# Kernel optimization log

Measured on AMD Instinct MI355X. Metric: run time of the kernel, lower is better.

Reference implementation:

```python
import jax, jax.numpy as jnp
import numpy as np

RADIUS = 0.1
KSIZE = 3          # kernel points per dimension
P_DIM = 3
K = KSIZE ** P_DIM  # 27 kernel points
KP_EXTENT = RADIUS / (KSIZE - 1) * P_DIM ** 0.5


def _kernel_points():
    # grid kernel points, same as getKernelPoints(radius, 3, dim=3)
    xyz = np.linspace(-1.0, 1.0, KSIZE)
    pts = np.meshgrid(*P_DIM * [xyz])
    pts = np.vstack([p.flatten() for p in pts]).T
    pts = pts / P_DIM ** 0.5
    return jnp.asarray(pts * RADIUS, dtype=jnp.float32)  # [K, 3]


def setup_inputs() -> dict:
    key = jax.random.key(0)
    k1, k2, k3, k4, k5 = jax.random.split(key, 5)
    N, S, H, CIN, COUT = 40000, 40000, 32, 64, 64
    # points in a [0, 0.2]^3 cube so neighbor offsets are comparable to radius
    q_pts = jax.random.uniform(k1, (N, 3), jnp.float32) * 0.2
    s_pts = jax.random.uniform(k2, (S, 3), jnp.float32) * 0.2
    neighb_inds = jax.random.randint(k3, (N, H), 0, S)
    x = jax.random.normal(k4, (S, CIN), jnp.float32)
    # kaiming-style init for the [K, Cin, Cout] grouped weights
    weights = jax.random.normal(k5, (K, CIN, COUT), jnp.float32) * (1.0 / np.sqrt(CIN))
    return {"q_pts": q_pts, "s_pts": s_pts, "neighb_inds": neighb_inds,
            "x": x, "weights": weights}


def reference(q_pts, s_pts, neighb_inds, x, weights):
    kp = _kernel_points()  # [K, 3], non-trainable constant
    # shadow padding row (sentinel point far away, zero feature)
    s_pad = jnp.concatenate([s_pts, jnp.full((1, s_pts.shape[-1]), 1e6, s_pts.dtype)], axis=0)
    x_pad = jnp.concatenate([x, jnp.zeros((1, x.shape[-1]), x.dtype)], axis=0)
    neighbors = s_pad[neighb_inds] - q_pts[:, None, :]      # [N, H, 3]
    neighb_x = x_pad[neighb_inds]                           # [N, H, Cin]
    # kernel-point influence weights: linear correlation clipped at 0
    diff = neighbors[:, :, None, :] - kp[None, None, :, :]  # [N, H, K, 3]
    sq_dist = jnp.sum(diff * diff, axis=-1)                 # [N, H, K]
    all_w = jnp.maximum(1.0 - jnp.sqrt(sq_dist) / KP_EXTENT, 0.0)
    # weighted grouped matmul over K kernel weight matrices
    fx = jnp.einsum('nhl,nhi,lio->no', all_w, neighb_x, weights)  # [N, Cout]
    return fx
```

## Files before the change

kernel.cpp:

```cpp
#include <hip/hip_runtime.h>

typedef _Float16 half_t;
typedef __fp16   fp16x2 __attribute__((ext_vector_type(2)));
typedef _Float16 half4_t __attribute__((ext_vector_type(4)));
typedef _Float16 half8   __attribute__((ext_vector_type(8)));
typedef float    f32x4   __attribute__((ext_vector_type(4)));
typedef unsigned short u16x8 __attribute__((ext_vector_type(8)));

#define KP_S    0.057735026918962574f
#define INV_EXT 11.547005383792515f
#define GPITCH  3616
#define NBLK    512
#define NTILE   2500
#define WT_BYTES (64 * 1792 * 2)
#define XH_BYTES (40000 * 64 * 2)

union H8 { half8 v; fp16x2 h2[4]; };
union H4 { half4_t v; fp16x2 h2[2]; };

__global__ void build_wt(const float* __restrict__ W, half_t* __restrict__ WT) {
    int t = blockIdx.x * 256 + threadIdx.x;
    if (t >= 64 * 1792) return;
    int o = t / 1792, k = t - o * 1792;
    int i = k / 28,   l = k - i * 28;
    int c = 4 * (i & 15) + (i >> 4);
    WT[t] = (l < 27) ? (half_t)W[(l * 64 + c) * 64 + o] : (half_t)0.f;
}

__global__ void build_xh(const float* __restrict__ x, half_t* __restrict__ xh) {
    int t = blockIdx.x * 256 + threadIdx.x;
    f32x4 v = *(const f32x4*)(x + t * 4);
    H4 h;
    h.h2[0] = __builtin_amdgcn_cvt_pkrtz(v.x, v.y);
    h.h2[1] = __builtin_amdgcn_cvt_pkrtz(v.z, v.w);
    *(half4_t*)(xh + t * 4) = h.v;
}

#define ISSUE_XV1(BUF, Q, XV) do {                                             \
    u16x8 id8 = *(const u16x8*)&idx_lds[BUF][Q][8 * g];                        \
    _Pragma("unroll")                                                          \
    for (int j = 0; j < 8; ++j) {                                              \
        if constexpr (XHALF) {                                                 \
            XV[j] = *(const half4_t*)(xh + (int)id8[j] * 64 + 4 * lr);         \
        } else {                                                               \
            f32x4 t4 = *(const f32x4*)(x + (int)id8[j] * 64 + 4 * lr);         \
            H4 hh;                                                             \
            hh.h2[0] = __builtin_amdgcn_cvt_pkrtz(t4.x, t4.y);                 \
            hh.h2[1] = __builtin_amdgcn_cvt_pkrtz(t4.z, t4.w);                 \
            XV[j] = hh.v;                                                      \
        }                                                                      \
    }                                                                          \
} while (0)

#define PACK_B(XV, BF) do {                                                    \
    _Pragma("unroll")                                                          \
    for (int nt = 0; nt < 4; ++nt) {                                           \
        half8 b;                                                               \
        _Pragma("unroll")                                                      \
        for (int j = 0; j < 8; ++j) b[j] = XV[j][nt];                          \
        BF[nt].v = b;                                                          \
    }                                                                          \
} while (0)

#define MFMA_DUMP(Q, CUR, BF) do {                                             \
    float w0v[8], w1v[8];                                                      \
    _Pragma("unroll")                                                          \
    for (int j = 0; j < 8; ++j) {                                              \
        f32x4 nb = nbr_lds[CUR][Q][8 * g + j];                                 \
        float dx = nb.x - kx0, dy = nb.y - ky0, dz = nb.z - kz0;               \
        w0v[j] = fmaxf(fmaf(__builtin_amdgcn_sqrtf(dx*dx + dy*dy + dz*dz), -INV_EXT, 1.f), 0.f); \
        float ex = nb.x - kx1, ey = nb.y - ky1, ez = nb.z - kz1;               \
        w1v[j] = fmaxf(fmaf(__builtin_amdgcn_sqrtf(ex*ex + ey*ey + ez*ez), -INV_EXT, cbias), 0.f); \
    }                                                                          \
    H8 A0, A1;                                                                 \
    _Pragma("unroll")                                                          \
    for (int p = 0; p < 4; ++p) {                                              \
        A0.h2[p] = __builtin_amdgcn_cvt_pkrtz(w0v[2*p], w0v[2*p+1]);           \
        A1.h2[p] = __builtin_amdgcn_cvt_pkrtz(w1v[2*p], w1v[2*p+1]);           \
    }                                                                          \
    char* gq = g_mem + (Q) * GPITCH;                                           \
    _Pragma("unroll")                                                          \
    for (int nt = 0; nt < 4; ++nt) {                                           \
        f32x4 z = {0.f, 0.f, 0.f, 0.f};                                        \
        f32x4 c0 = __builtin_amdgcn_mfma_f32_16x16x32_f16(A0.v, BF[nt].v, z, 0, 0, 0); \
        f32x4 c1 = __builtin_amdgcn_mfma_f32_16x16x32_f16(A1.v, BF[nt].v, z, 0, 0, 0); \
        const int ic = 16 * nt + lr;                                           \
        H4 h0;                                                                 \
        h0.h2[0] = __builtin_amdgcn_cvt_pkrtz(c0[0], c0[1]);                   \
        h0.h2[1] = __builtin_amdgcn_cvt_pkrtz(c0[2], c0[3]);                   \
        *(half4_t*)(gq + 2 * (ic * 28 + 4 * g)) = h0.v;                        \
        if (4 * g < 12) {                                                      \
            H4 h1;                                                             \
            h1.h2[0] = __builtin_amdgcn_cvt_pkrtz(c1[0], c1[1]);               \
            h1.h2[1] = __builtin_amdgcn_cvt_pkrtz(c1[2], c1[3]);               \
            *(half4_t*)(gq + 2 * (ic * 28 + 16 + 4 * g)) = h1.v;               \
        }                                                                      \
    }                                                                          \
} while (0)

#define BODY(T, TN, CUR, XV) do {                                              \
              \
    half4_t xvB[8];                                                            \
    ISSUE_XV1(CUR, 2 * wid + 1, xvB);                                          \
    H8 BFA[4];                                                                 \
    PACK_B(XV, BFA);                                                           \
    const int nn   = (TN) * 16 + aq;                                           \
    const int idxN = inds[nn * 32 + ah];                                       \
    MFMA_DUMP(2 * wid, CUR, BFA);                                              \
    f32x4 vN;                                                                  \
    vN.x = s_pts[idxN * 3 + 0] - q_pts[nn * 3 + 0];                            \
    vN.y = s_pts[idxN * 3 + 1] - q_pts[nn * 3 + 1];                            \
    vN.z = s_pts[idxN * 3 + 2] - q_pts[nn * 3 + 2];                            \
    vN.w = 0.f;                                                                \
    H8 BFB[4];                                                                 \
    PACK_B(xvB, BFB);                                                          \
    MFMA_DUMP(2 * wid + 1, CUR, BFB);                                          \
    idx_lds[(CUR) ^ 1][aq][ah] = (unsigned short)idxN;                         \
    nbr_lds[(CUR) ^ 1][aq][ah] = vN;                                           \
    __syncthreads();                                                           \
                              \
    ISSUE_XV1((CUR) ^ 1, 2 * wid, XV);                                         \
             \
    const half_t* wrow = WT + (16 * ot + lr) * 1792 + kh * 896 + 8 * g;        \
    const char*   gb   = g_mem + lr * GPITCH + kh * 1792;                      \
    f32x4 accA = {0.f, 0.f, 0.f, 0.f}, accB = {0.f, 0.f, 0.f, 0.f};            \
    _Pragma("unroll 7")                                                        \
    for (int s = 0; s < 28; s += 2) {                                          \
        half8 aA = *(const half8*)(gb + 64 * s + 16 * g);                      \
        half8 bA = *(const half8*)(wrow + 32 * s);                             \
        accA = __builtin_amdgcn_mfma_f32_16x16x32_f16(aA, bA, accA, 0, 0, 0);  \
        half8 aB = *(const half8*)(gb + 64 * (s + 1) + 16 * g);                \
        half8 bB = *(const half8*)(wrow + 32 * (s + 1));                       \
        accB = __builtin_amdgcn_mfma_f32_16x16x32_f16(aB, bB, accB, 0, 0, 0);  \
    }                                                                          \
    f32x4 acc = accA + accB;                                                   \
    if (kh) *(f32x4*)&red[ot][lane] = acc;                                     \
    __syncthreads();                                                           \
    if (!kh) {                                                                 \
        f32x4 p = red[ot][lane];                                               \
        const int o = 16 * ot + lr;                                            \
        _Pragma("unroll")                                                      \
        for (int r = 0; r < 4; ++r)                                            \
            out[((T) * 16 + 4 * g + r) * 64 + o] = acc[r] + p[r];              \
    }                                                                          \
} while (0)

template <int XHALF>
__global__ __launch_bounds__(512, 4) void kpconv(
    const float* __restrict__ q_pts, const float* __restrict__ s_pts,
    const int*   __restrict__ inds,  const float* __restrict__ x,
    const half_t* __restrict__ xh,   const half_t* __restrict__ WT,
    float* __restrict__ out)
{
    __shared__ __align__(16) char   g_mem[16 * GPITCH];
    __shared__ __align__(16) unsigned short idx_lds[2][16][32];
    __shared__ __align__(16) f32x4  nbr_lds[2][16][32];
    __shared__ __align__(16) f32x4  red[4][64];

    const int tid  = threadIdx.x;
    const int lane = tid & 63, wid = tid >> 6;
    const int lr   = lane & 15, g = lane >> 4;
    const int aq   = tid >> 5,  ah = tid & 31;
    const int ot   = wid & 3,   kh = wid >> 2;

    const float kx0 = (float)((lr / 3) % 3 - 1) * KP_S;
    const float ky0 = (float)( lr / 9      - 1) * KP_S;
    const float kz0 = (float)( lr % 3      - 1) * KP_S;
    const int   l1  = lr + 16;
    const float kx1 = (float)((l1 / 3) % 3 - 1) * KP_S;
    const float ky1 = (float)( l1 / 9      - 1) * KP_S;
    const float kz1 = (float)( l1 % 3      - 1) * KP_S;
    const float cbias = (l1 < 27) ? 1.f : -1.f;

    {
        int n   = blockIdx.x * 16 + aq;
        int idx = inds[n * 32 + ah];
        idx_lds[0][aq][ah] = (unsigned short)idx;
        f32x4 v;
        v.x = s_pts[idx * 3 + 0] - q_pts[n * 3 + 0];
        v.y = s_pts[idx * 3 + 1] - q_pts[n * 3 + 1];
        v.z = s_pts[idx * 3 + 2] - q_pts[n * 3 + 2];
        v.w = 0.f;
        nbr_lds[0][aq][ah] = v;
    }
    __syncthreads();

    half4_t xv[8];
    ISSUE_XV1(0, 2 * wid, xv);

    int cur = 0;
    for (int t = blockIdx.x; t < NTILE; t += NBLK) {
        int tn = (t + NBLK < NTILE) ? t + NBLK : t;
        BODY(t, tn, cur, xv);
        cur ^= 1;
    }
}

extern "C" void kernel_launch(void* const* d_in, const int* in_sizes, int n_in,
                              void* d_out, int out_size, void* d_ws, size_t ws_size,
                              hipStream_t stream) {
    const float* q_pts = (const float*)d_in[0];
    const float* s_pts = (const float*)d_in[1];
    const int*   inds  = (const int*)d_in[2];
    const float* x     = (const float*)d_in[3];
    const float* W     = (const float*)d_in[4];
    float* out = (float*)d_out;
    half_t* WT = (half_t*)d_ws;
    half_t* xh = (half_t*)((char*)d_ws + WT_BYTES);

    build_wt<<<448, 256, 0, stream>>>(W, WT);
    if (ws_size >= (size_t)(WT_BYTES + XH_BYTES)) {
        build_xh<<<2500, 256, 0, stream>>>(x, xh);
        kpconv<1><<<NBLK, 512, 0, stream>>>(q_pts, s_pts, inds, x, xh, WT, out);
    } else {
        kpconv<0><<<NBLK, 512, 0, stream>>>(q_pts, s_pts, inds, x, xh, WT, out);
    }
}
```

Before: 97.23 us.

## Double block tile to 32 points with 1024 threads and fp16 neighbor offsets

Each block now processes 32 query points per tile with 1024 threads (16 waves), split across two M-halves, so every weight row loaded from global is reused across twice as many outputs. Neighbor offsets are stored in LDS as packed fp16 instead of float4, halving that buffer's footprint. Barriers are replaced with an explicit lgkmcnt wait plus s_barrier. The trade-offs are lower precision in the offset distances, more LDS per block (which may limit occupancy), and fewer blocks in the grid.

Result: slower. 108.7 us (+11.8%).

```diff
diff --git a/kernel.cpp b/kernel.cpp
--- a/kernel.cpp
+++ b/kernel.cpp
@@ -10,13 +10,18 @@
 #define KP_S    0.057735026918962574f
 #define INV_EXT 11.547005383792515f
 #define GPITCH  3616
-#define NBLK    512
-#define NTILE   2500
+#define NBLK    256
+#define NTILE   1250
 #define WT_BYTES (64 * 1792 * 2)
 #define XH_BYTES (40000 * 64 * 2)
 
 union H8 { half8 v; fp16x2 h2[4]; };
 union H4 { half4_t v; fp16x2 h2[2]; };
+
+#define BAR_LGKM() do {                                                        \
+    __asm__ volatile("s_waitcnt lgkmcnt(0)\n\ts_barrier" ::: "memory");        \
+    __builtin_amdgcn_sched_barrier(0);                                         \
+} while (0)
 
 __global__ void build_wt(const float* __restrict__ W, half_t* __restrict__ WT) {
     int t = blockIdx.x * 256 + threadIdx.x;
@@ -66,10 +71,11 @@
     float w0v[8], w1v[8];                                                      \
     _Pragma("unroll")                                                          \
     for (int j = 0; j < 8; ++j) {                                              \
-        f32x4 nb = nbr_lds[CUR][Q][8 * g + j];                                 \
-        float dx = nb.x - kx0, dy = nb.y - ky0, dz = nb.z - kz0;               \
+        half4_t nb = nbr_lds[CUR][Q][8 * g + j];                               \
+        float nx = (float)nb[0], ny = (float)nb[1], nz = (float)nb[2];         \
+        float dx = nx - kx0, dy = ny - ky0, dz = nz - kz0;                     \
         w0v[j] = fmaxf(fmaf(__builtin_amdgcn_sqrtf(dx*dx + dy*dy + dz*dz), -INV_EXT, 1.f), 0.f); \
-        float ex = nb.x - kx1, ey = nb.y - ky1, ez = nb.z - kz1;               \
+        float ex = nx - kx1, ey = ny - ky1, ez = nz - kz1;                     \
         w1v[j] = fmaxf(fmaf(__builtin_amdgcn_sqrtf(ex*ex + ey*ey + ez*ez), -INV_EXT, cbias), 0.f); \
     }                                                                          \
     H8 A0, A1;                                                                 \
@@ -104,25 +110,26 @@
     ISSUE_XV1(CUR, 2 * wid + 1, xvB);                                          \
     H8 BFA[4];                                                                 \
     PACK_B(XV, BFA);                                                           \
-    const int nn   = (TN) * 16 + aq;                                           \
+    const int nn   = (TN) * 32 + aq;                                           \
     const int idxN = inds[nn * 32 + ah];                                       \
     MFMA_DUMP(2 * wid, CUR, BFA);                                              \
-    f32x4 vN;                                                                  \
-    vN.x = s_pts[idxN * 3 + 0] - q_pts[nn * 3 + 0];                            \
-    vN.y = s_pts[idxN * 3 + 1] - q_pts[nn * 3 + 1];                            \
-    vN.z = s_pts[idxN * 3 + 2] - q_pts[nn * 3 + 2];                            \
-    vN.w = 0.f;                                                                \
+    const float sx = s_pts[idxN * 3 + 0] - q_pts[nn * 3 + 0];                  \
+    const float sy = s_pts[idxN * 3 + 1] - q_pts[nn * 3 + 1];                  \
+    const float sz = s_pts[idxN * 3 + 2] - q_pts[nn * 3 + 2];                  \
     H8 BFB[4];                                                                 \
     PACK_B(xvB, BFB);                                                          \
     MFMA_DUMP(2 * wid + 1, CUR, BFB);                                          \
     idx_lds[(CUR) ^ 1][aq][ah] = (unsigned short)idxN;                         \
-    nbr_lds[(CUR) ^ 1][aq][ah] = vN;                                           \
-    __syncthreads();                                                           \
+    { H4 nv;                                                                   \
+      nv.h2[0] = __builtin_amdgcn_cvt_pkrtz(sx, sy);                           \
+      nv.h2[1] = __builtin_amdgcn_cvt_pkrtz(sz, 0.f);                          \
+      nbr_lds[(CUR) ^ 1][aq][ah] = nv.v; }                                     \
+    BAR_LGKM();                                                                \
                               \
     ISSUE_XV1((CUR) ^ 1, 2 * wid, XV);                                         \
              \
     const half_t* wrow = WT + (16 * ot + lr) * 1792 + kh * 896 + 8 * g;        \
-    const char*   gb   = g_mem + lr * GPITCH + kh * 1792;                      \
+    const char*   gb   = g_mem + (16 * mh + lr) * GPITCH + kh * 1792;          \
     f32x4 accA = {0.f, 0.f, 0.f, 0.f}, accB = {0.f, 0.f, 0.f, 0.f};            \
     _Pragma("unroll 7")                                                        \
     for (int s = 0; s < 28; s += 2) {                                          \
@@ -134,34 +141,36 @@
         accB = __builtin_amdgcn_mfma_f32_16x16x32_f16(aB, bB, accB, 0, 0, 0);  \
     }                                                                          \
     f32x4 acc = accA + accB;                                                   \
-    if (kh) *(f32x4*)&red[ot][lane] = acc;                                     \
-    __syncthreads();                                                           \
+    if (kh) *(f32x4*)&red[mh][ot][lane] = acc;                                 \
+    BAR_LGKM();                                                                \
     if (!kh) {                                                                 \
-        f32x4 p = red[ot][lane];                                               \
+        f32x4 p = red[mh][ot][lane];                                           \
         const int o = 16 * ot + lr;                                            \
         _Pragma("unroll")                                                      \
         for (int r = 0; r < 4; ++r)                                            \
-            out[((T) * 16 + 4 * g + r) * 64 + o] = acc[r] + p[r];              \
+            out[((T) * 32 + 16 * mh + 4 * g + r) * 64 + o] = acc[r] + p[r];    \
     }                                                                          \
 } while (0)
 
 template <int XHALF>
-__global__ __launch_bounds__(512, 4) void kpconv(
+__global__ __launch_bounds__(1024) void kpconv(
     const float* __restrict__ q_pts, const float* __restrict__ s_pts,
     const int*   __restrict__ inds,  const float* __restrict__ x,
     const half_t* __restrict__ xh,   const half_t* __restrict__ WT,
     float* __restrict__ out)
 {
-    __shared__ __align__(16) char   g_mem[16 * GPITCH];
-    __shared__ __align__(16) unsigned short idx_lds[2][16][32];
-    __shared__ __align__(16) f32x4  nbr_lds[2][16][32];
-    __shared__ __align__(16) f32x4  red[4][64];
+    __shared__ __align__(16) char    g_mem[32 * GPITCH];
+    __shared__ __align__(16) unsigned short idx_lds[2][32][32];
+    __shared__ __align__(16) half4_t nbr_lds[2][32][32];
+    __shared__ __align__(16) f32x4   red[2][4][64];
 
     const int tid  = threadIdx.x;
     const int lane = tid & 63, wid = tid >> 6;
     const int lr   = lane & 15, g = lane >> 4;
     const int aq   = tid >> 5,  ah = tid & 31;
-    const int ot   = wid & 3,   kh = wid >> 2;
+    const int ot   = wid & 3;
+    const int mh   = (wid >> 2) & 1;
+    const int kh   = wid >> 3;
 
     const float kx0 = (float)((lr / 3) % 3 - 1) * KP_S;
     const float ky0 = (float)( lr / 9      - 1) * KP_S;
@@ -173,15 +182,16 @@
     const float cbias = (l1 < 27) ? 1.f : -1.f;
 
     {
-        int n   = blockIdx.x * 16 + aq;
+        int n   = blockIdx.x * 32 + aq;
         int idx = inds[n * 32 + ah];
         idx_lds[0][aq][ah] = (unsigned short)idx;
-        f32x4 v;
-        v.x = s_pts[idx * 3 + 0] - q_pts[n * 3 + 0];
-        v.y = s_pts[idx * 3 + 1] - q_pts[n * 3 + 1];
-        v.z = s_pts[idx * 3 + 2] - q_pts[n * 3 + 2];
-        v.w = 0.f;
-        nbr_lds[0][aq][ah] = v;
+        float dx = s_pts[idx * 3 + 0] - q_pts[n * 3 + 0];
+        float dy = s_pts[idx * 3 + 1] - q_pts[n * 3 + 1];
+        float dz = s_pts[idx * 3 + 2] - q_pts[n * 3 + 2];
+        H4 nv;
+        nv.h2[0] = __builtin_amdgcn_cvt_pkrtz(dx, dy);
+        nv.h2[1] = __builtin_amdgcn_cvt_pkrtz(dz, 0.f);
+        nbr_lds[0][aq][ah] = nv.v;
     }
     __syncthreads();
 
@@ -211,8 +221,8 @@
     build_wt<<<448, 256, 0, stream>>>(W, WT);
     if (ws_size >= (size_t)(WT_BYTES + XH_BYTES)) {
         build_xh<<<2500, 256, 0, stream>>>(x, xh);
-        kpconv<1><<<NBLK, 512, 0, stream>>>(q_pts, s_pts, inds, x, xh, WT, out);
+        kpconv<1><<<NBLK, 1024, 0, stream>>>(q_pts, s_pts, inds, x, xh, WT, out);
     } else {
-        kpconv<0><<<NBLK, 512, 0, stream>>>(q_pts, s_pts, inds, x, xh, WT, out);
+        kpconv<0><<<NBLK, 1024, 0, stream>>>(q_pts, s_pts, inds, x, xh, WT, out);
     }
 }
```

## Store neighbor offsets as fp16, prefetch indices two tiles ahead, cache weights in registers

Applied to the files above, without the earlier changes.

Adds a pre-pass that converts query and support points to padded fp16 quads, so each neighbor offset is one 8-byte gather and an fp16 subtract. The LDS neighbor buffer shrinks to half4. Neighbor indices are prefetched one extra tile ahead in a register to hide gather latency. The first 7 weight fragments of the grouped matmul stay in registers across tiles, and the reduction loop is restructured. The trade-offs are lower precision on the offsets, higher register pressure under the 512x4 launch bound, and an extra small kernel launch.

After: 120.2 us. 23.6% more time.

```diff
diff --git a/kernel.cpp b/kernel.cpp
--- a/kernel.cpp
+++ b/kernel.cpp
@@ -14,6 +14,7 @@
 #define NTILE   2500
 #define WT_BYTES (64 * 1792 * 2)
 #define XH_BYTES (40000 * 64 * 2)
+#define PH_BYTES (40000 * 4 * 2)
 
 union H8 { half8 v; fp16x2 h2[4]; };
 union H4 { half4_t v; fp16x2 h2[2]; };
@@ -34,6 +35,19 @@
     h.h2[0] = __builtin_amdgcn_cvt_pkrtz(v.x, v.y);
     h.h2[1] = __builtin_amdgcn_cvt_pkrtz(v.z, v.w);
     *(half4_t*)(xh + t * 4) = h.v;
+}
+
+__global__ void build_ph(const float* __restrict__ q_pts, const float* __restrict__ s_pts,
+                         half_t* __restrict__ qh, half_t* __restrict__ sh) {
+    int i = blockIdx.x * 256 + threadIdx.x;
+    if (i >= 40000) return;
+    H4 a, b;
+    a.h2[0] = __builtin_amdgcn_cvt_pkrtz(q_pts[3*i], q_pts[3*i+1]);
+    a.h2[1] = __builtin_amdgcn_cvt_pkrtz(q_pts[3*i+2], 0.f);
+    b.h2[0] = __builtin_amdgcn_cvt_pkrtz(s_pts[3*i], s_pts[3*i+1]);
+    b.h2[1] = __builtin_amdgcn_cvt_pkrtz(s_pts[3*i+2], 0.f);
+    *(half4_t*)(qh + 4*i) = a.v;
+    *(half4_t*)(sh + 4*i) = b.v;
 }
 
 #define ISSUE_XV1(BUF, Q, XV) do {                                             \
@@ -65,12 +79,17 @@
 #define MFMA_DUMP(Q, CUR, BF) do {                                             \
     float w0v[8], w1v[8];                                                      \
     _Pragma("unroll")                                                          \
-    for (int j = 0; j < 8; ++j) {                                              \
-        f32x4 nb = nbr_lds[CUR][Q][8 * g + j];                                 \
-        float dx = nb.x - kx0, dy = nb.y - ky0, dz = nb.z - kz0;               \
-        w0v[j] = fmaxf(fmaf(__builtin_amdgcn_sqrtf(dx*dx + dy*dy + dz*dz), -INV_EXT, 1.f), 0.f); \
-        float ex = nb.x - kx1, ey = nb.y - ky1, ez = nb.z - kz1;               \
-        w1v[j] = fmaxf(fmaf(__builtin_amdgcn_sqrtf(ex*ex + ey*ey + ez*ez), -INV_EXT, cbias), 0.f); \
+    for (int j2 = 0; j2 < 4; ++j2) {                                           \
+        half8 nb2 = *(const half8*)&nbr_lds[CUR][Q][8 * g + 2 * j2];           \
+        _Pragma("unroll")                                                      \
+        for (int u = 0; u < 2; ++u) {                                          \
+            const int j = 2 * j2 + u;                                          \
+            float nx = (float)nb2[4*u+0], ny = (float)nb2[4*u+1], nz = (float)nb2[4*u+2]; \
+            float dx = nx - kx0, dy = ny - ky0, dz = nz - kz0;                 \
+            w0v[j] = fmaxf(fmaf(__builtin_amdgcn_sqrtf(dx*dx + dy*dy + dz*dz), -INV_EXT, 1.f), 0.f); \
+            float ex = nx - kx1, ey = ny - ky1, ez = nz - kz1;                 \
+            w1v[j] = fmaxf(fmaf(__builtin_amdgcn_sqrtf(ex*ex + ey*ey + ez*ez), -INV_EXT, cbias), 0.f); \
+        }                                                                      \
     }                                                                          \
     H8 A0, A1;                                                                 \
     _Pragma("unroll")                                                          \
@@ -98,40 +117,51 @@
     }                                                                          \
 } while (0)
 
-#define BODY(T, TN, CUR, XV) do {                                              \
+#define BODY(T, TNN, CUR, XV) do {                                             \
               \
     half4_t xvB[8];                                                            \
     ISSUE_XV1(CUR, 2 * wid + 1, xvB);                                          \
+    const int idxN = idxReg;                         \
+    idxReg = inds[((TNN) * 16 + aq) * 32 + ah];     \
     H8 BFA[4];                                                                 \
     PACK_B(XV, BFA);                                                           \
-    const int nn   = (TN) * 16 + aq;                                           \
-    const int idxN = inds[nn * 32 + ah];                                       \
     MFMA_DUMP(2 * wid, CUR, BFA);                                              \
-    f32x4 vN;                                                                  \
-    vN.x = s_pts[idxN * 3 + 0] - q_pts[nn * 3 + 0];                            \
-    vN.y = s_pts[idxN * 3 + 1] - q_pts[nn * 3 + 1];                            \
-    vN.z = s_pts[idxN * 3 + 2] - q_pts[nn * 3 + 2];                            \
-    vN.w = 0.f;                                                                \
+         \
+    half4_t nv;                                                                \
+    if constexpr (PH) {                                                        \
+        half4_t sv = *(const half4_t*)(sh + 4 * idxN);                         \
+        half4_t qv = *(const half4_t*)(qh + 4 * nnq);                          \
+        nv = sv - qv;                                                          \
+    } else {                                                                   \
+        float dx = s_pts[idxN*3+0] - q_pts[nnq*3+0];                           \
+        float dy = s_pts[idxN*3+1] - q_pts[nnq*3+1];                           \
+        float dz = s_pts[idxN*3+2] - q_pts[nnq*3+2];                           \
+        H4 t;                                                                  \
+        t.h2[0] = __builtin_amdgcn_cvt_pkrtz(dx, dy);                          \
+        t.h2[1] = __builtin_amdgcn_cvt_pkrtz(dz, 0.f);                         \
+        nv = t.v;                                                              \
+    }                                                                          \
     H8 BFB[4];                                                                 \
     PACK_B(xvB, BFB);                                                          \
     MFMA_DUMP(2 * wid + 1, CUR, BFB);                                          \
     idx_lds[(CUR) ^ 1][aq][ah] = (unsigned short)idxN;                         \
-    nbr_lds[(CUR) ^ 1][aq][ah] = vN;                                           \
+    nbr_lds[(CUR) ^ 1][aq][ah] = nv;                                           \
     __syncthreads();                                                           \
                               \
     ISSUE_XV1((CUR) ^ 1, 2 * wid, XV);                                         \
-             \
-    const half_t* wrow = WT + (16 * ot + lr) * 1792 + kh * 896 + 8 * g;        \
-    const char*   gb   = g_mem + lr * GPITCH + kh * 1792;                      \
+        \
     f32x4 accA = {0.f, 0.f, 0.f, 0.f}, accB = {0.f, 0.f, 0.f, 0.f};            \
-    _Pragma("unroll 7")                                                        \
-    for (int s = 0; s < 28; s += 2) {                                          \
-        half8 aA = *(const half8*)(gb + 64 * s + 16 * g);                      \
-        half8 bA = *(const half8*)(wrow + 32 * s);                             \
-        accA = __builtin_amdgcn_mfma_f32_16x16x32_f16(aA, bA, accA, 0, 0, 0);  \
-        half8 aB = *(const half8*)(gb + 64 * (s + 1) + 16 * g);                \
-        half8 bB = *(const half8*)(wrow + 32 * (s + 1));                       \
-        accB = __builtin_amdgcn_mfma_f32_16x16x32_f16(aB, bB, accB, 0, 0, 0);  \
+    _Pragma("unroll")                                                          \
+    for (int s = 0; s < 7; ++s) {                                              \
+        half8 a = *(const half8*)(gb + 64 * s + 16 * g);                       \
+        accA = __builtin_amdgcn_mfma_f32_16x16x32_f16(a, wreg[s], accA, 0, 0, 0); \
+    }                                                                          \
+    _Pragma("unroll")                                                          \
+    for (int s = 7; s < 28; ++s) {                                             \
+        half8 a = *(const half8*)(gb + 64 * s + 16 * g);                       \
+        half8 b = *(const half8*)(wrow + 32 * s);                              \
+        if (s & 1) accB = __builtin_amdgcn_mfma_f32_16x16x32_f16(a, b, accB, 0, 0, 0); \
+        else       accA = __builtin_amdgcn_mfma_f32_16x16x32_f16(a, b, accA, 0, 0, 0); \
     }                                                                          \
     f32x4 acc = accA + accB;                                                   \
     if (kh) *(f32x4*)&red[ot][lane] = acc;                                     \
@@ -145,17 +175,18 @@
     }                                                                          \
 } while (0)
 
-template <int XHALF>
+template <int XHALF, int PH>
 __global__ __launch_bounds__(512, 4) void kpconv(
     const float* __restrict__ q_pts, const float* __restrict__ s_pts,
     const int*   __restrict__ inds,  const float* __restrict__ x,
-    const half_t* __restrict__ xh,   const half_t* __restrict__ WT,
+    const half_t* __restrict__ xh,   const half_t* __restrict__ sh,
+    const half_t* __restrict__ qh,   const half_t* __restrict__ WT,
     float* __restrict__ out)
 {
-    __shared__ __align__(16) char   g_mem[16 * GPITCH];
+    __shared__ __align__(16) char    g_mem[16 * GPITCH];
     __shared__ __align__(16) unsigned short idx_lds[2][16][32];
-    __shared__ __align__(16) f32x4  nbr_lds[2][16][32];
-    __shared__ __align__(16) f32x4  red[4][64];
+    __shared__ __align__(16) half4_t nbr_lds[2][16][32];
+    __shared__ __align__(16) f32x4   red[4][64];
 
     const int tid  = threadIdx.x;
     const int lane = tid & 63, wid = tid >> 6;
@@ -172,26 +203,37 @@
     const float kz1 = (float)( l1 % 3      - 1) * KP_S;
     const float cbias = (l1 < 27) ? 1.f : -1.f;
 
+    const half_t* wrow = WT + (16 * ot + lr) * 1792 + kh * 896 + 8 * g;
+    const char*   gb   = g_mem + lr * GPITCH + kh * 1792;
+    half8 wreg[7];
+    #pragma unroll
+    for (int p = 0; p < 7; ++p) wreg[p] = *(const half8*)(wrow + 32 * p);
+
     {
         int n   = blockIdx.x * 16 + aq;
         int idx = inds[n * 32 + ah];
         idx_lds[0][aq][ah] = (unsigned short)idx;
-        f32x4 v;
-        v.x = s_pts[idx * 3 + 0] - q_pts[n * 3 + 0];
-        v.y = s_pts[idx * 3 + 1] - q_pts[n * 3 + 1];
-        v.z = s_pts[idx * 3 + 2] - q_pts[n * 3 + 2];
-        v.w = 0.f;
-        nbr_lds[0][aq][ah] = v;
+        float dx = s_pts[idx * 3 + 0] - q_pts[n * 3 + 0];
+        float dy = s_pts[idx * 3 + 1] - q_pts[n * 3 + 1];
+        float dz = s_pts[idx * 3 + 2] - q_pts[n * 3 + 2];
+        H4 nv;
+        nv.h2[0] = __builtin_amdgcn_cvt_pkrtz(dx, dy);
+        nv.h2[1] = __builtin_amdgcn_cvt_pkrtz(dz, 0.f);
+        nbr_lds[0][aq][ah] = nv.v;
     }
     __syncthreads();
 
     half4_t xv[8];
     ISSUE_XV1(0, 2 * wid, xv);
+    const int t1 = (blockIdx.x + NBLK < NTILE) ? blockIdx.x + NBLK : blockIdx.x;
+    int idxReg = inds[(t1 * 16 + aq) * 32 + ah];
 
     int cur = 0;
     for (int t = blockIdx.x; t < NTILE; t += NBLK) {
-        int tn = (t + NBLK < NTILE) ? t + NBLK : t;
-        BODY(t, tn, cur, xv);
+        const int tn  = (t + NBLK < NTILE) ? t + NBLK : t;
+        const int tnn = (t + 2 * NBLK < NTILE) ? t + 2 * NBLK : tn;
+        const int nnq = tn * 16 + aq;
+        BODY(t, tnn, cur, xv);
         cur ^= 1;
     }
 }
@@ -207,12 +249,20 @@
     float* out = (float*)d_out;
     half_t* WT = (half_t*)d_ws;
     half_t* xh = (half_t*)((char*)d_ws + WT_BYTES);
+    half_t* sh = (half_t*)((char*)d_ws + WT_BYTES + XH_BYTES);
+    half_t* qh = (half_t*)((char*)d_ws + WT_BYTES + XH_BYTES + PH_BYTES);
 
     build_wt<<<448, 256, 0, stream>>>(W, WT);
-    if (ws_size >= (size_t)(WT_BYTES + XH_BYTES)) {
+    const size_t need_xh   = (size_t)WT_BYTES + XH_BYTES;
+    const size_t need_full = need_xh + 2 * (size_t)PH_BYTES;
+    if (ws_size >= need_full) {
         build_xh<<<2500, 256, 0, stream>>>(x, xh);
-        kpconv<1><<<NBLK, 512, 0, stream>>>(q_pts, s_pts, inds, x, xh, WT, out);
+        build_ph<<<157, 256, 0, stream>>>(q_pts, s_pts, qh, sh);
+        kpconv<1, 1><<<NBLK, 512, 0, stream>>>(q_pts, s_pts, inds, x, xh, sh, qh, WT, out);
+    } else if (ws_size >= need_xh) {
+        build_xh<<<2500, 256, 0, stream>>>(x, xh);
+        kpconv<1, 0><<<NBLK, 512, 0, stream>>>(q_pts, s_pts, inds, x, xh, sh, qh, WT, out);
     } else {
-        kpconv<0><<<NBLK, 512, 0, stream>>>(q_pts, s_pts, inds, x, xh, WT, out);
+        kpconv<0, 0><<<NBLK, 512, 0, stream>>>(q_pts, s_pts, inds, x, xh, sh, qh, WT, out);
     }
 }
```

## Split fused KPConv into gather-weight kernel and dense weight-matmul kernel

Applied to the files above, without the earlier changes.

When the workspace is large enough, the persistent fused kernel is replaced by two kernels. The first writes a per-point intermediate G (kernel-point-weighted neighbor features, fp16) to global memory. The second runs a dense MFMA matmul of G against a re-laid-out weight matrix, split across four waves with an LDS reduction. This removes the LDS staging and the intra-block sync pipeline, but adds a round trip of roughly 143 MB of G through global memory.

Result: slower. 132.3 us (+36.1%).

```diff
diff --git a/kernel.cpp b/kernel.cpp
--- a/kernel.cpp
+++ b/kernel.cpp
@@ -9,23 +9,18 @@
 
 #define KP_S    0.057735026918962574f
 #define INV_EXT 11.547005383792515f
-#define GPITCH  3616
-#define NBLK    512
 #define NTILE   2500
 #define WT_BYTES (64 * 1792 * 2)
 #define XH_BYTES (40000 * 64 * 2)
+#define G_BYTES  (40000 * 3584)
+#define GROW     3584
+
+#define GPITCH  3616
+#define NBLK_F  512
 
 union H8 { half8 v; fp16x2 h2[4]; };
 union H4 { half4_t v; fp16x2 h2[2]; };
 
-__global__ void build_wt(const float* __restrict__ W, half_t* __restrict__ WT) {
-    int t = blockIdx.x * 256 + threadIdx.x;
-    if (t >= 64 * 1792) return;
-    int o = t / 1792, k = t - o * 1792;
-    int i = k / 28,   l = k - i * 28;
-    int c = 4 * (i & 15) + (i >> 4);
-    WT[t] = (l < 27) ? (half_t)W[(l * 64 + c) * 64 + o] : (half_t)0.f;
-}
 
 __global__ void build_xh(const float* __restrict__ x, half_t* __restrict__ xh) {
     int t = blockIdx.x * 256 + threadIdx.x;
@@ -35,6 +30,175 @@
     h.h2[1] = __builtin_amdgcn_cvt_pkrtz(v.z, v.w);
     *(half4_t*)(xh + t * 4) = h.v;
 }
+
+__global__ void build_wt_split(const float* __restrict__ W, half_t* __restrict__ WT) {
+    int t = blockIdx.x * 256 + threadIdx.x;
+    if (t >= 64 * 1792) return;
+    int o = t / 1792, k = t - o * 1792;
+    int l, i;
+    if (k < 1024) {
+        int nt = k >> 8, m = (k >> 2) & 63, r = k & 3;
+        l = 4 * (m >> 4) + r;  i = 16 * nt + (m & 15);
+    } else {
+        int u = k - 1024;
+        int nt = u / 192, v = u - nt * 192;
+        int m = v >> 2, r = v & 3;
+        l = 16 + 4 * (m >> 4) + r;  i = 16 * nt + (m & 15);
+    }
+    int c = 4 * (i & 15) + (i >> 4);
+    WT[t] = (half_t)W[(l * 64 + c) * 64 + o];
+}
+
+__global__ void build_wt_fused(const float* __restrict__ W, half_t* __restrict__ WT) {
+    int t = blockIdx.x * 256 + threadIdx.x;
+    if (t >= 64 * 1792) return;
+    int o = t / 1792, k = t - o * 1792;
+    int i = k / 28,   l = k - i * 28;
+    int c = 4 * (i & 15) + (i >> 4);
+    WT[t] = (l < 27) ? (half_t)W[(l * 64 + c) * 64 + o] : (half_t)0.f;
+}
+
+__global__ __launch_bounds__(512, 4) void kpconvA(
+    const float* __restrict__ q_pts, const float* __restrict__ s_pts,
+    const int*   __restrict__ inds,  const half_t* __restrict__ xh,
+    half_t* __restrict__ G)
+{
+    __shared__ __align__(16) unsigned short idx_lds[16][32];
+    __shared__ __align__(16) f32x4 nbr_lds[16][32];
+
+    const int tid  = threadIdx.x;
+    const int lane = tid & 63, wid = tid >> 6;
+    const int lr   = lane & 15, g = lane >> 4;
+    const int aq   = tid >> 5,  ah = tid & 31;
+    const int base = blockIdx.x * 16;
+
+    const float kx0 = (float)((lr / 3) % 3 - 1) * KP_S;
+    const float ky0 = (float)( lr / 9      - 1) * KP_S;
+    const float kz0 = (float)( lr % 3      - 1) * KP_S;
+    const int   l1  = lr + 16;
+    const float kx1 = (float)((l1 / 3) % 3 - 1) * KP_S;
+    const float ky1 = (float)( l1 / 9      - 1) * KP_S;
+    const float kz1 = (float)( l1 % 3      - 1) * KP_S;
+    const float cbias = (l1 < 27) ? 1.f : -1.f;
+
+    {
+        int n   = base + aq;
+        int idx = inds[n * 32 + ah];
+        idx_lds[aq][ah] = (unsigned short)idx;
+        f32x4 v;
+        v.x = s_pts[idx * 3 + 0] - q_pts[n * 3 + 0];
+        v.y = s_pts[idx * 3 + 1] - q_pts[n * 3 + 1];
+        v.z = s_pts[idx * 3 + 2] - q_pts[n * 3 + 2];
+        v.w = 0.f;
+        nbr_lds[aq][ah] = v;
+    }
+    __syncthreads();
+
+    half4_t xvA[8], xvB[8];
+    {
+        u16x8 idA = *(const u16x8*)&idx_lds[2 * wid][8 * g];
+        u16x8 idB = *(const u16x8*)&idx_lds[2 * wid + 1][8 * g];
+        #pragma unroll
+        for (int j = 0; j < 8; ++j) {
+            xvA[j] = *(const half4_t*)(xh + (int)idA[j] * 64 + 4 * lr);
+            xvB[j] = *(const half4_t*)(xh + (int)idB[j] * 64 + 4 * lr);
+        }
+    }
+
+    #pragma unroll
+    for (int qq = 0; qq < 2; ++qq) {
+        const int q = 2 * wid + qq;
+        float w0v[8], w1v[8];
+        #pragma unroll
+        for (int j = 0; j < 8; ++j) {
+            f32x4 nb = nbr_lds[q][8 * g + j];
+            float dx = nb.x - kx0, dy = nb.y - ky0, dz = nb.z - kz0;
+            w0v[j] = fmaxf(fmaf(__builtin_amdgcn_sqrtf(dx*dx + dy*dy + dz*dz), -INV_EXT, 1.f), 0.f);
+            float ex = nb.x - kx1, ey = nb.y - ky1, ez = nb.z - kz1;
+            w1v[j] = fmaxf(fmaf(__builtin_amdgcn_sqrtf(ex*ex + ey*ey + ez*ez), -INV_EXT, cbias), 0.f);
+        }
+        H8 A0, A1;
+        #pragma unroll
+        for (int p = 0; p < 4; ++p) {
+            A0.h2[p] = __builtin_amdgcn_cvt_pkrtz(w0v[2*p], w0v[2*p+1]);
+            A1.h2[p] = __builtin_amdgcn_cvt_pkrtz(w1v[2*p], w1v[2*p+1]);
+        }
+        char* gq = (char*)G + (size_t)(base + q) * GROW;
+        #pragma unroll
+        for (int nt = 0; nt < 4; ++nt) {
+            half8 b;
+            #pragma unroll
+            for (int j = 0; j < 8; ++j) b[j] = (qq ? xvB : xvA)[j][nt];
+            f32x4 z = {0.f, 0.f, 0.f, 0.f};
+            f32x4 c0 = __builtin_amdgcn_mfma_f32_16x16x32_f16(A0.v, b, z, 0, 0, 0);
+            f32x4 c1 = __builtin_amdgcn_mfma_f32_16x16x32_f16(A1.v, b, z, 0, 0, 0);
+            H4 h0;
+            h0.h2[0] = __builtin_amdgcn_cvt_pkrtz(c0[0], c0[1]);
+            h0.h2[1] = __builtin_amdgcn_cvt_pkrtz(c0[2], c0[3]);
+            *(half4_t*)(gq + nt * 512 + lane * 8) = h0.v;
+            if (g < 3) {
+                H4 h1;
+                h1.h2[0] = __builtin_amdgcn_cvt_pkrtz(c1[0], c1[1]);
+                h1.h2[1] = __builtin_amdgcn_cvt_pkrtz(c1[2], c1[3]);
+                *(half4_t*)(gq + 2048 + nt * 384 + lane * 8) = h1.v;
+            }
+        }
+    }
+}
+
+__global__ __launch_bounds__(256, 6) void kpconvB(
+    const half_t* __restrict__ G, const half_t* __restrict__ WT,
+    float* __restrict__ out)
+{
+    __shared__ __align__(16) f32x4 red[3][4][64];
+
+    const int tid  = threadIdx.x;
+    const int lane = tid & 63, kq = tid >> 6;
+    const int lr   = lane & 15, g = lane >> 4;
+    const int base = blockIdx.x * 16;
+
+    const char* ga = (const char*)G + (size_t)(base + lr) * GROW + kq * 896 + 16 * g;
+
+    f32x4 acc0 = {0,0,0,0}, acc1 = {0,0,0,0}, acc2 = {0,0,0,0}, acc3 = {0,0,0,0};
+    const half_t* w0 = WT + (lr     ) * 1792 + kq * 448 + 8 * g;
+    const half_t* w1 = WT + (lr + 16) * 1792 + kq * 448 + 8 * g;
+    const half_t* w2 = WT + (lr + 32) * 1792 + kq * 448 + 8 * g;
+    const half_t* w3 = WT + (lr + 48) * 1792 + kq * 448 + 8 * g;
+    #pragma unroll
+    for (int s = 0; s < 14; ++s) {
+        half8 a = *(const half8*)(ga + 64 * s);
+        half8 b0 = *(const half8*)(w0 + 32 * s);
+        half8 b1 = *(const half8*)(w1 + 32 * s);
+        half8 b2 = *(const half8*)(w2 + 32 * s);
+        half8 b3 = *(const half8*)(w3 + 32 * s);
+        acc0 = __builtin_amdgcn_mfma_f32_16x16x32_f16(a, b0, acc0, 0, 0, 0);
+        acc1 = __builtin_amdgcn_mfma_f32_16x16x32_f16(a, b1, acc1, 0, 0, 0);
+        acc2 = __builtin_amdgcn_mfma_f32_16x16x32_f16(a, b2, acc2, 0, 0, 0);
+        acc3 = __builtin_amdgcn_mfma_f32_16x16x32_f16(a, b3, acc3, 0, 0, 0);
+    }
+    if (kq) {
+        *(f32x4*)&red[kq - 1][0][lane] = acc0;
+        *(f32x4*)&red[kq - 1][1][lane] = acc1;
+        *(f32x4*)&red[kq - 1][2][lane] = acc2;
+        *(f32x4*)&red[kq - 1][3][lane] = acc3;
+    }
+    __syncthreads();
+    if (kq == 0) {
+        f32x4 r0 = acc0 + red[0][0][lane] + red[1][0][lane] + red[2][0][lane];
+        f32x4 r1 = acc1 + red[0][1][lane] + red[1][1][lane] + red[2][1][lane];
+        f32x4 r2 = acc2 + red[0][2][lane] + red[1][2][lane] + red[2][2][lane];
+        f32x4 r3 = acc3 + red[0][3][lane] + red[1][3][lane] + red[2][3][lane];
+        #pragma unroll
+        for (int r = 0; r < 4; ++r) {
+            float* orow = out + (base + 4 * g + r) * 64 + lr;
+            orow[ 0] = r0[r];
+            orow[16] = r1[r];
+            orow[32] = r2[r];
+            orow[48] = r3[r];
+        }
+    }
+}
+
 
 #define ISSUE_XV1(BUF, Q, XV) do {                                             \
     u16x8 id8 = *(const u16x8*)&idx_lds[BUF][Q][8 * g];                        \
@@ -99,7 +263,6 @@
 } while (0)
 
 #define BODY(T, TN, CUR, XV) do {                                              \
-              \
     half4_t xvB[8];                                                            \
     ISSUE_XV1(CUR, 2 * wid + 1, xvB);                                          \
     H8 BFA[4];                                                                 \
@@ -118,9 +281,7 @@
     idx_lds[(CUR) ^ 1][aq][ah] = (unsigned short)idxN;                         \
     nbr_lds[(CUR) ^ 1][aq][ah] = vN;                                           \
     __syncthreads();                                                           \
-                              \
     ISSUE_XV1((CUR) ^ 1, 2 * wid, XV);                                         \
-             \
     const half_t* wrow = WT + (16 * ot + lr) * 1792 + kh * 896 + 8 * g;        \
     const char*   gb   = g_mem + lr * GPITCH + kh * 1792;                      \
     f32x4 accA = {0.f, 0.f, 0.f, 0.f}, accB = {0.f, 0.f, 0.f, 0.f};            \
@@ -146,7 +307,7 @@
 } while (0)
 
 template <int XHALF>
-__global__ __launch_bounds__(512, 4) void kpconv(
+__global__ __launch_bounds__(512, 4) void kpconv_fused(
     const float* __restrict__ q_pts, const float* __restrict__ s_pts,
     const int*   __restrict__ inds,  const float* __restrict__ x,
     const half_t* __restrict__ xh,   const half_t* __restrict__ WT,
@@ -189,12 +350,13 @@
     ISSUE_XV1(0, 2 * wid, xv);
 
     int cur = 0;
-    for (int t = blockIdx.x; t < NTILE; t += NBLK) {
-        int tn = (t + NBLK < NTILE) ? t + NBLK : t;
+    for (int t = blockIdx.x; t < NTILE; t += NBLK_F) {
+        int tn = (t + NBLK_F < NTILE) ? t + NBLK_F : t;
         BODY(t, tn, cur, xv);
         cur ^= 1;
     }
 }
+
 
 extern "C" void kernel_launch(void* const* d_in, const int* in_sizes, int n_in,
                               void* d_out, int out_size, void* d_ws, size_t ws_size,
@@ -207,12 +369,22 @@
     float* out = (float*)d_out;
     half_t* WT = (half_t*)d_ws;
     half_t* xh = (half_t*)((char*)d_ws + WT_BYTES);
-
-    build_wt<<<448, 256, 0, stream>>>(W, WT);
-    if (ws_size >= (size_t)(WT_BYTES + XH_BYTES)) {
+    half_t* G  = (half_t*)((char*)d_ws + WT_BYTES + XH_BYTES);
+
+    const size_t need_split = (size_t)WT_BYTES + XH_BYTES + G_BYTES;
+    const size_t need_xh    = (size_t)WT_BYTES + XH_BYTES;
+
+    if (ws_size >= need_split) {
+        build_wt_split<<<448, 256, 0, stream>>>(W, WT);
         build_xh<<<2500, 256, 0, stream>>>(x, xh);
-        kpconv<1><<<NBLK, 512, 0, stream>>>(q_pts, s_pts, inds, x, xh, WT, out);
+        kpconvA<<<2500, 512, 0, stream>>>(q_pts, s_pts, inds, xh, G);
+        kpconvB<<<2500, 256, 0, stream>>>(G, WT, out);
+    } else if (ws_size >= need_xh) {
+        build_wt_fused<<<448, 256, 0, stream>>>(W, WT);
+        build_xh<<<2500, 256, 0, stream>>>(x, xh);
+        kpconv_fused<1><<<NBLK_F, 512, 0, stream>>>(q_pts, s_pts, inds, x, xh, WT, out);
     } else {
-        kpconv<0><<<NBLK, 512, 0, stream>>>(q_pts, s_pts, inds, x, xh, WT, out);
-    }
-}
+        build_wt_fused<<<448, 256, 0, stream>>>(W, WT);
+        kpconv_fused<0><<<NBLK_F, 512, 0, stream>>>(q_pts, s_pts, inds, x, xh, WT, out);
+    }
+}
```
